# Kernel tuning notes

Measured on AMD Instinct MI355X. Metric: run time of the kernel, lower is better.

Reference implementation:

```python
import jax, jax.numpy as jnp
import numpy as np

EMBED = 512
HEADS = 8
HEAD_DIM = EMBED // HEADS


def setup_inputs() -> dict:
    key = jax.random.key(0)
    k1, k2, k3, k4 = jax.random.split(key, 4)
    B, S = 2, 4096
    return {
        "query": jax.random.normal(k1, (B, S, EMBED), dtype=jnp.float32),
        "key": jax.random.normal(k2, (B, S, EMBED), dtype=jnp.float32),
        "value": jax.random.normal(k3, (B, S, EMBED), dtype=jnp.float32),
        "Wo": jax.random.normal(k4, (EMBED, EMBED), dtype=jnp.float32) / np.sqrt(EMBED),
        "bo": jnp.zeros((EMBED,), dtype=jnp.float32),
        "mask": 1,
    }


def reference(query, key, value, Wo, bo, mask):
    B, Sq, _ = query.shape
    Sk = key.shape[1]
    # [B, H, S, D] via reshape + permute (matches torch module)
    q = query.reshape(B, Sq, HEADS, HEAD_DIM).transpose(0, 2, 1, 3)
    k = key.reshape(B, Sk, HEADS, HEAD_DIM).transpose(0, 2, 1, 3)
    v = value.reshape(B, Sk, HEADS, HEAD_DIM).transpose(0, 2, 1, 3)
    scale = 1.0 / jnp.sqrt(jnp.float32(HEAD_DIM))
    scores = jnp.einsum("bhqd,bhkd->bhqk", q, k) * scale  # [B,H,Sq,Sk]
    if mask is not None:
        # additive -inf strictly above diagonal (causal), as torch.triu(full(-inf), 1)
        causal = jnp.triu(jnp.full((Sq, Sk), -jnp.inf, dtype=scores.dtype), k=1)
        scores = scores + causal
    attn = jax.nn.softmax(scores, axis=-1)
    out = jnp.einsum("bhqk,bhkd->bhqd", attn, v)
    out = out.transpose(0, 2, 1, 3).reshape(B, Sq, HEADS * HEAD_DIM)
    return out @ Wo.T + bo
```

## Files before the change

kernel.cpp:

```cpp
#include <hip/hip_runtime.h>
#include <hip/hip_bf16.h>
#include <math.h>

#define SDIM 4096
#define EMB 512
#define NH 8
#define HD 64
#define QBLK 128
#define KVB 64
#define NB 2
#define NQT (SDIM / QBLK)
#define NPAIR (NQT / 2)

typedef __attribute__((ext_vector_type(4)))  float f32x4;
typedef __attribute__((ext_vector_type(16))) float f32x16;
typedef __attribute__((ext_vector_type(8)))  short bf16x8;
typedef __attribute__((ext_vector_type(4)))  unsigned u32x4;

#define SCQ 0.18033688011112042f
#define THR 8.0f

__device__ __forceinline__ unsigned cvt_pk(float lo, float hi) {
    unsigned r;
    asm("v_cvt_pk_bf16_f32 %0, %1, %2" : "=v"(r) : "v"(lo), "v"(hi));
    return r;
}
__device__ __forceinline__ void pl32swap(unsigned &a, unsigned &b) {
    asm("v_permlane32_swap_b32 %0, %1" : "+v"(a), "+v"(b));
}

__global__ __launch_bounds__(512) void attn_fwd(
    const float* __restrict__ Q, const float* __restrict__ K,
    const float* __restrict__ V, short* __restrict__ X)
{
    __shared__ short smem[32768];
    __shared__ float mlb[4][32][2];

    int bh   = blockIdx.x & 15;
    int pair = blockIdx.x >> 4;
    int b = bh / NH, h = bh % NH;

    int tid  = threadIdx.x;
    int wave = tid >> 6, lane = tid & 63;
    int team = wave >> 2, w = wave & 3;
    int ln = lane & 31, hi = lane >> 5;
    int swz = 8 * (ln & 7);
    int shbase = 36 * hi;

    int ttid = tid & 255;
    const int kr = ttid >> 2, kc = (ttid & 3) * 16;
    const int vp = ttid & 31, vdb = (ttid >> 5) * 8;

    f32x4 pk0, pk1, pk2, pk3, pv0, pv1, pv2, pv3;

    auto ISSUE = [&](int k0) {
        const float* kp = K + ((size_t)(b * SDIM + k0 + kr)) * EMB + h * HD + kc;
        pk0 = *(const f32x4*)(kp + 0);
        pk1 = *(const f32x4*)(kp + 4);
        pk2 = *(const f32x4*)(kp + 8);
        pk3 = *(const f32x4*)(kp + 12);
        const float* v0p = V + ((size_t)(b * SDIM + k0 + 2 * vp)) * EMB + h * HD + vdb;
        pv0 = *(const f32x4*)(v0p);
        pv1 = *(const f32x4*)(v0p + 4);
        pv2 = *(const f32x4*)(v0p + EMB);
        pv3 = *(const f32x4*)(v0p + EMB + 4);
    };

    auto WRITE_STAGE = [&](int buf) {
        short* Klp = &smem[(team * 2 + buf) * 8192];
        short* Vtp = Klp + 4096;
        int rs = 8 * (kr & 7);
        u32x4 w0 = { cvt_pk(pk0[0],pk0[1]), cvt_pk(pk0[2],pk0[3]),
                     cvt_pk(pk1[0],pk1[1]), cvt_pk(pk1[2],pk1[3]) };
        u32x4 w1 = { cvt_pk(pk2[0],pk2[1]), cvt_pk(pk2[2],pk2[3]),
                     cvt_pk(pk3[0],pk3[1]), cvt_pk(pk3[2],pk3[3]) };
        *(u32x4*)&Klp[kr * HD + ((kc + 0) ^ rs)] = w0;
        *(u32x4*)&Klp[kr * HD + ((kc + 8) ^ rs)] = w1;
        unsigned* vt32 = (unsigned*)Vtp;
#pragma unroll
        for (int i = 0; i < 4; ++i) {
            int d = vdb + i;
            vt32[d * 32 + (vp ^ (4 * (d & 7)))] = cvt_pk(pv0[i], pv2[i]);
        }
#pragma unroll
        for (int i = 0; i < 4; ++i) {
            int d = vdb + 4 + i;
            vt32[d * 32 + (vp ^ (4 * (d & 7)))] = cvt_pk(pv1[i], pv3[i]);
        }
    };

    bf16x8 qf0, qf1, qf2, qf3;
    float m2, l_run;
    f32x16 accO0, accO1;
    int qbase, q_g;

    auto LOAD_Q = [&]() {
        const float* qp = Q + ((size_t)(b * SDIM + q_g)) * EMB + h * HD + 8 * hi;
#pragma unroll
        for (int s = 0; s < 4; ++s) {
            f32x4 a = *(const f32x4*)(qp + 16 * s) * SCQ;
            f32x4 c = *(const f32x4*)(qp + 16 * s + 4) * SCQ;
            u32x4 wq = { cvt_pk(a[0], a[1]), cvt_pk(a[2], a[3]),
                         cvt_pk(c[0], c[1]), cvt_pk(c[2], c[3]) };
            bf16x8 f = (bf16x8)wq;
            if (s == 0) qf0 = f; else if (s == 1) qf1 = f;
            else if (s == 2) qf2 = f; else qf3 = f;
        }
    };

    auto COMPUTE = [&](int buf, int k0) {
        short* Klp = &smem[(team * 2 + buf) * 8192];
        short* Vtp = Klp + 4096;
        float p0[16], p1[16];
#pragma unroll
        for (int t = 0; t < 2; ++t) {
            f32x16 acc = (f32x16){0.f,0.f,0.f,0.f,0.f,0.f,0.f,0.f,
                                  0.f,0.f,0.f,0.f,0.f,0.f,0.f,0.f};
            __builtin_amdgcn_s_setprio(1);
#pragma unroll
            for (int s = 0; s < 4; ++s) {
                bf16x8 kf = *(bf16x8*)&Klp[(32*t + ln) * HD + ((16*s + 8*hi) ^ swz)];
                bf16x8 qs = (s == 0) ? qf0 : (s == 1) ? qf1 : (s == 2) ? qf2 : qf3;
                acc = __builtin_amdgcn_mfma_f32_32x32x16_bf16(kf, qs, acc, 0, 0, 0);
            }
            __builtin_amdgcn_s_setprio(0);
            float* pt = t ? p1 : p0;
            if (k0 + 32*t + 31 > qbase) {
#pragma unroll
                for (int r = 0; r < 16; ++r) {
                    int kv = k0 + 32*t + (r & 3) + 8*(r >> 2) + 4*hi;
                    pt[r] = (kv > q_g) ? -INFINITY : acc[r];
                }
            } else {
#pragma unroll
                for (int r = 0; r < 16; ++r) pt[r] = acc[r];
            }
        }

        float mx[16];
#pragma unroll
        for (int r = 0; r < 16; ++r) mx[r] = fmaxf(p0[r], p1[r]);
#pragma unroll
        for (int r = 0; r < 8; ++r) mx[r] = fmaxf(mx[r], mx[r + 8]);
#pragma unroll
        for (int r = 0; r < 4; ++r) mx[r] = fmaxf(mx[r], mx[r + 4]);
        float mt = fmaxf(fmaxf(mx[0], mx[1]), fmaxf(mx[2], mx[3]));
        mt = fmaxf(mt, __shfl_xor(mt, 32, 64));

        if (!__all(mt <= m2 + THR)) {
            float m_new = fmaxf(m2, mt);
            float fac = __builtin_amdgcn_exp2f(m2 - m_new);
            m2 = m_new;
            l_run *= fac;
#pragma unroll
            for (int r = 0; r < 16; ++r) {
                float fr = __shfl(fac, shbase + ((r & 3) + 8*(r >> 2)), 64);
                accO0[r] *= fr;
                accO1[r] *= fr;
            }
        }
        float sm[16];
#pragma unroll
        for (int r = 0; r < 16; ++r) {
            p0[r] = __builtin_amdgcn_exp2f(p0[r] - m2);
            p1[r] = __builtin_amdgcn_exp2f(p1[r] - m2);
            sm[r] = p0[r] + p1[r];
        }
#pragma unroll
        for (int r = 0; r < 8; ++r) sm[r] += sm[r + 8];
#pragma unroll
        for (int r = 0; r < 4; ++r) sm[r] += sm[r + 4];
        float psum = (sm[0] + sm[1]) + (sm[2] + sm[3]);
        psum += __shfl_xor(psum, 32, 64);
        l_run += psum;

#pragma unroll
        for (int s = 0; s < 4; ++s) {
            const float* pt = (s >= 2) ? p1 : p0;
            const int u8 = (s & 1) * 8;
            unsigned w0 = cvt_pk(pt[u8 + 0], pt[u8 + 1]);
            unsigned w2 = cvt_pk(pt[u8 + 4], pt[u8 + 5]);
            pl32swap(w0, w2);
            unsigned w1 = cvt_pk(pt[u8 + 2], pt[u8 + 3]);
            unsigned w3 = cvt_pk(pt[u8 + 6], pt[u8 + 7]);
            pl32swap(w1, w3);
            u32x4 pw = { w0, w1, w2, w3 };
            bf16x8 pa = (bf16x8)pw;
            bf16x8 v0f = *(bf16x8*)&Vtp[(ln)      * KVB + ((16*s + 8*hi) ^ swz)];
            bf16x8 v1f = *(bf16x8*)&Vtp[(32 + ln) * KVB + ((16*s + 8*hi) ^ swz)];
            __builtin_amdgcn_s_setprio(1);
            accO0 = __builtin_amdgcn_mfma_f32_32x32x16_bf16(pa, v0f, accO0, 0, 0, 0);
            accO1 = __builtin_amdgcn_mfma_f32_32x32x16_bf16(pa, v1f, accO1, 0, 0, 0);
            __builtin_amdgcn_s_setprio(0);
        }
    };

    auto FINISH = [&]() {
        __syncthreads();
        f32x4* O4 = (f32x4*)&smem[16384];
        if (team == 1) {
            if (hi == 0) { mlb[w][ln][0] = m2; mlb[w][ln][1] = l_run; }
#pragma unroll
            for (int rq = 0; rq < 4; ++rq)
                O4[(w * 8 + rq) * 64 + lane] =
                    (f32x4){accO0[4*rq], accO0[4*rq+1], accO0[4*rq+2], accO0[4*rq+3]};
#pragma unroll
            for (int rq = 0; rq < 4; ++rq)
                O4[(w * 8 + 4 + rq) * 64 + lane] =
                    (f32x4){accO1[4*rq], accO1[4*rq+1], accO1[4*rq+2], accO1[4*rq+3]};
        }
        __syncthreads();
        if (team == 0) {
            float mB = mlb[w][ln][0], lB = mlb[w][ln][1];
            float m  = fmaxf(m2, mB);
            float aS = __builtin_amdgcn_exp2f(m2 - m);
            float bS = __builtin_amdgcn_exp2f(mB - m);
            float il = 1.f / (l_run * aS + lB * bS);
            float fa = aS * il, fb = bS * il;
            f32x4 ob[8];
#pragma unroll
            for (int rq = 0; rq < 8; ++rq) ob[rq] = O4[(w * 8 + rq) * 64 + lane];
#pragma unroll
            for (int r = 0; r < 16; ++r) {
                int crow = (r & 3) + 8 * (r >> 2);
                float faR = __shfl(fa, shbase + crow, 64);
                float fbR = __shfl(fb, shbase + crow, 64);
                float o0 = accO0[r] * faR + ob[r >> 2][r & 3] * fbR;
                float o1 = accO1[r] * faR + ob[4 + (r >> 2)][r & 3] * fbR;
                int q = qbase + crow + 4 * hi;
                size_t base = ((size_t)(b * SDIM + q)) * EMB + h * HD;
                X[base + ln]      = (short)cvt_pk(o0, 0.f);
                X[base + 32 + ln] = (short)cvt_pk(o1, 0.f);
            }
        }
        __syncthreads();
    };

    auto RUN_SEG = [&](int qt) {
        qbase = qt * QBLK + w * 32;
        q_g = qbase + ln;
        LOAD_Q();
        m2 = -1e30f; l_run = 0.f;
        accO0 = (f32x16){0.f,0.f,0.f,0.f,0.f,0.f,0.f,0.f,0.f,0.f,0.f,0.f,0.f,0.f,0.f,0.f};
        accO1 = accO0;
        const int nt  = 2 * qt + 2;
        const int cnt = nt >> 1;
        ISSUE(team * KVB);
        for (int i = 0; i < cnt; ++i) {
            int buf = i & 1;
            WRITE_STAGE(buf);
            int tn = 2 * (i + 1) + team;
            if (tn < nt) ISSUE(tn * KVB);
            __builtin_amdgcn_sched_barrier(0);
            __syncthreads();
            int k0 = (2 * i + team) * KVB;
            if (k0 <= qbase + 31) COMPUTE(buf, k0);
        }
        FINISH();
    };

    RUN_SEG(NQT - 1 - pair);
    RUN_SEG(pair);
}

__global__ __launch_bounds__(256, 2) void proj_gemm(
    const short* __restrict__ X, const float* __restrict__ Wo,
    const float* __restrict__ bo, float* __restrict__ out)
{
    __shared__ short Alds[64][40];
    __shared__ short Blds[64][40];

    int bj = blockIdx.x & 7;
    int bi = blockIdx.x >> 3;
    int i0 = bi * 64, j0 = bj * 64;

    int tid  = threadIdx.x;
    int wave = tid >> 6, lane = tid & 63;
    int g = lane >> 4, ln = lane & 15;
    int srow = tid >> 2, scol = (tid & 3) * 8;

    f32x4 acc[4];
#pragma unroll
    for (int i = 0; i < 4; ++i) acc[i] = (f32x4){0.f, 0.f, 0.f, 0.f};

    for (int e0 = 0; e0 < EMB; e0 += 32) {
        bf16x8 xa = *(const bf16x8*)&X[(size_t)(i0 + srow) * EMB + e0 + scol];
        *(bf16x8*)&Alds[srow][scol] = xa;

        const float* wp = Wo + (size_t)(j0 + srow) * EMB + e0 + scol;
        f32x4 a = *(const f32x4*)wp;
        f32x4 c = *(const f32x4*)(wp + 4);
        u32x4 w = { cvt_pk(a[0], a[1]), cvt_pk(a[2], a[3]),
                    cvt_pk(c[0], c[1]), cvt_pk(c[2], c[3]) };
        *(u32x4*)&Blds[srow][scol] = w;
        __syncthreads();

        bf16x8 af = *(bf16x8*)&Alds[wave * 16 + ln][g * 8];
#pragma unroll
        for (int nt = 0; nt < 4; ++nt) {
            bf16x8 bf = *(bf16x8*)&Blds[nt * 16 + ln][g * 8];
            acc[nt] = __builtin_amdgcn_mfma_f32_16x16x32_bf16(af, bf, acc[nt], 0, 0, 0);
        }
        __syncthreads();
    }

#pragma unroll
    for (int nt = 0; nt < 4; ++nt)
#pragma unroll
        for (int r = 0; r < 4; ++r) {
            int row = i0 + wave * 16 + g * 4 + r;
            int col = j0 + nt * 16 + ln;
            out[(size_t)row * EMB + col] = acc[nt][r] + bo[col];
        }
}

extern "C" void kernel_launch(void* const* d_in, const int* in_sizes, int n_in,
                              void* d_out, int out_size, void* d_ws, size_t ws_size,
                              hipStream_t stream) {
    const float* Q  = (const float*)d_in[0];
    const float* K  = (const float*)d_in[1];
    const float* V  = (const float*)d_in[2];
    const float* Wo = (const float*)d_in[3];
    const float* bo = (const float*)d_in[4];
    short* X   = (short*)d_ws;
    float* out = (float*)d_out;

    attn_fwd<<<dim3(NB * NH * NPAIR), 512, 0, stream>>>(Q, K, V, X);
    proj_gemm<<<dim3((NB * SDIM / 64) * (EMB / 64)), 256, 0, stream>>>(X, Wo, bo, out);
}
```

Baseline: 97.83 us.

## Split causal KV loop across four wave teams with tree merge

Doubles the attention block to 1024 threads, organised as four teams of four waves. The KV tiles of each query segment are striped across the four teams, shortening each team's serial loop. The partial softmax states are then combined with a two-level tree merge through shared memory, which is doubled to hold the extra staging buffers and partial outputs. The cost is more LDS per block, extra barriers and merge work, and the tighter launch bounds may force register spills.

Result: slower. 236.8 us (+142.0%).

```diff
diff --git a/kernel.cpp b/kernel.cpp
--- a/kernel.cpp
+++ b/kernel.cpp
@@ -29,12 +29,12 @@
     asm("v_permlane32_swap_b32 %0, %1" : "+v"(a), "+v"(b));
 }
 
-__global__ __launch_bounds__(512) void attn_fwd(
+__global__ __launch_bounds__(1024, 4) void attn_fwd(
     const float* __restrict__ Q, const float* __restrict__ K,
     const float* __restrict__ V, short* __restrict__ X)
 {
-    __shared__ short smem[32768];
-    __shared__ float mlb[4][32][2];
+    __shared__ __align__(16) short smem[65536];
+    __shared__ float mlb[4][4][32][2];
 
     int bh   = blockIdx.x & 15;
     int pair = blockIdx.x >> 4;
@@ -195,44 +195,65 @@
         }
     };
 
+    auto STORE_O = [&](float* R) {
+        f32x4* O4 = (f32x4*)R;
+#pragma unroll
+        for (int rq = 0; rq < 4; ++rq)
+            O4[(w * 8 + rq) * 64 + lane] =
+                (f32x4){accO0[4*rq], accO0[4*rq+1], accO0[4*rq+2], accO0[4*rq+3]};
+#pragma unroll
+        for (int rq = 0; rq < 4; ++rq)
+            O4[(w * 8 + 4 + rq) * 64 + lane] =
+                (f32x4){accO1[4*rq], accO1[4*rq+1], accO1[4*rq+2], accO1[4*rq+3]};
+    };
+
+    auto MERGE_FROM = [&](float* R, float (*mlp)[32][2]) {
+        float mB = mlp[w][ln][0], lB = mlp[w][ln][1];
+        float m  = fmaxf(m2, mB);
+        float aS = __builtin_amdgcn_exp2f(m2 - m);
+        float bS = __builtin_amdgcn_exp2f(mB - m);
+        l_run = l_run * aS + lB * bS;
+        m2 = m;
+        f32x4* O4 = (f32x4*)R;
+        f32x4 ob[8];
+#pragma unroll
+        for (int rq = 0; rq < 8; ++rq) ob[rq] = O4[(w * 8 + rq) * 64 + lane];
+#pragma unroll
+        for (int r = 0; r < 16; ++r) {
+            int crow = (r & 3) + 8 * (r >> 2);
+            float faR = __shfl(aS, shbase + crow, 64);
+            float fbR = __shfl(bS, shbase + crow, 64);
+            accO0[r] = accO0[r] * faR + ob[r >> 2][r & 3] * fbR;
+            accO1[r] = accO1[r] * faR + ob[4 + (r >> 2)][r & 3] * fbR;
+        }
+    };
+
+    auto WRITE_X = [&]() {
+        float il = 1.f / l_run;
+#pragma unroll
+        for (int r = 0; r < 16; ++r) {
+            int crow = (r & 3) + 8 * (r >> 2);
+            float ir = __shfl(il, shbase + crow, 64);
+            int q = qbase + crow + 4 * hi;
+            size_t base = ((size_t)(b * SDIM + q)) * EMB + h * HD;
+            X[base + ln]      = (short)cvt_pk(accO0[r] * ir, 0.f);
+            X[base + 32 + ln] = (short)cvt_pk(accO1[r] * ir, 0.f);
+        }
+    };
+
     auto FINISH = [&]() {
         __syncthreads();
-        f32x4* O4 = (f32x4*)&smem[16384];
-        if (team == 1) {
-            if (hi == 0) { mlb[w][ln][0] = m2; mlb[w][ln][1] = l_run; }
-#pragma unroll
-            for (int rq = 0; rq < 4; ++rq)
-                O4[(w * 8 + rq) * 64 + lane] =
-                    (f32x4){accO0[4*rq], accO0[4*rq+1], accO0[4*rq+2], accO0[4*rq+3]};
-#pragma unroll
-            for (int rq = 0; rq < 4; ++rq)
-                O4[(w * 8 + 4 + rq) * 64 + lane] =
-                    (f32x4){accO1[4*rq], accO1[4*rq+1], accO1[4*rq+2], accO1[4*rq+3]};
-        }
-        __syncthreads();
-        if (team == 0) {
-            float mB = mlb[w][ln][0], lB = mlb[w][ln][1];
-            float m  = fmaxf(m2, mB);
-            float aS = __builtin_amdgcn_exp2f(m2 - m);
-            float bS = __builtin_amdgcn_exp2f(mB - m);
-            float il = 1.f / (l_run * aS + lB * bS);
-            float fa = aS * il, fb = bS * il;
-            f32x4 ob[8];
-#pragma unroll
-            for (int rq = 0; rq < 8; ++rq) ob[rq] = O4[(w * 8 + rq) * 64 + lane];
-#pragma unroll
-            for (int r = 0; r < 16; ++r) {
-                int crow = (r & 3) + 8 * (r >> 2);
-                float faR = __shfl(fa, shbase + crow, 64);
-                float fbR = __shfl(fb, shbase + crow, 64);
-                float o0 = accO0[r] * faR + ob[r >> 2][r & 3] * fbR;
-                float o1 = accO1[r] * faR + ob[4 + (r >> 2)][r & 3] * fbR;
-                int q = qbase + crow + 4 * hi;
-                size_t base = ((size_t)(b * SDIM + q)) * EMB + h * HD;
-                X[base + ln]      = (short)cvt_pk(o0, 0.f);
-                X[base + 32 + ln] = (short)cvt_pk(o1, 0.f);
-            }
-        }
+        float* Of = (float*)smem;
+        if (hi == 0) { mlb[team][w][ln][0] = m2; mlb[team][w][ln][1] = l_run; }
+        if (team & 1) STORE_O(Of + (team >> 1) * 8192);
+        __syncthreads();
+        if ((team & 1) == 0) MERGE_FROM(Of + (team >> 1) * 8192, mlb[team + 1]);
+        if (team == 2) {
+            if (hi == 0) { mlb[2][w][ln][0] = m2; mlb[2][w][ln][1] = l_run; }
+            STORE_O(Of + 2 * 8192);
+        }
+        __syncthreads();
+        if (team == 0) { MERGE_FROM(Of + 2 * 8192, mlb[2]); WRITE_X(); }
         __syncthreads();
     };
 
@@ -243,18 +264,20 @@
         m2 = -1e30f; l_run = 0.f;
         accO0 = (f32x16){0.f,0.f,0.f,0.f,0.f,0.f,0.f,0.f,0.f,0.f,0.f,0.f,0.f,0.f,0.f,0.f};
         accO1 = accO0;
-        const int nt  = 2 * qt + 2;
-        const int cnt = nt >> 1;
-        ISSUE(team * KVB);
-        for (int i = 0; i < cnt; ++i) {
-            int buf = i & 1;
-            WRITE_STAGE(buf);
-            int tn = 2 * (i + 1) + team;
+        const int nt = 2 * qt + 2;
+        const int cm = (nt + 3) >> 2;
+        if (team < nt) ISSUE(team * KVB);
+        for (int it = 0; it < cm; ++it) {
+            int i = 4 * it + team;
+            if (i < nt) WRITE_STAGE(it & 1);
+            int tn = 4 * (it + 1) + team;
             if (tn < nt) ISSUE(tn * KVB);
             __builtin_amdgcn_sched_barrier(0);
             __syncthreads();
-            int k0 = (2 * i + team) * KVB;
-            if (k0 <= qbase + 31) COMPUTE(buf, k0);
+            if (i < nt) {
+                int k0 = i * KVB;
+                if (k0 <= qbase + 31) COMPUTE(it & 1, k0);
+            }
         }
         FINISH();
     };
@@ -325,6 +348,6 @@
     short* X   = (short*)d_ws;
     float* out = (float*)d_out;
 
-    attn_fwd<<<dim3(NB * NH * NPAIR), 512, 0, stream>>>(Q, K, V, X);
+    attn_fwd<<<dim3(NB * NH * NPAIR), 1024, 0, stream>>>(Q, K, V, X);
     proj_gemm<<<dim3((NB * SDIM / 64) * (EMB / 64)), 256, 0, stream>>>(X, Wo, bo, out);
 }
```
